# Performance work log

Measured on AMD Instinct MI355X. Metric: run time of the kernel, lower is better.

The kernel has to match this reference:

```python
import jax, jax.numpy as jnp
import numpy as np

D_MODEL = 1024
N_HEADS = 16
MLP_DIM = 4096


def _layernorm(x, g, b, eps=1e-5):
    mu = jnp.mean(x, axis=-1, keepdims=True)
    var = jnp.var(x, axis=-1, keepdims=True)
    return (x - mu) * jax.lax.rsqrt(var + eps) * g + b


def setup_inputs() -> dict:
    key = jax.random.key(0)
    ks = jax.random.split(key, 12)
    B, S, D, F = 2, 2048, D_MODEL, MLP_DIM
    s = 1.0 / np.sqrt(D)
    sf = 1.0 / np.sqrt(F)
    return {
        "x": jax.random.normal(ks[0], (B, S, D), jnp.float32),
        "ln1_g": jnp.ones((D,), jnp.float32),
        "ln1_b": jnp.zeros((D,), jnp.float32),
        "w_q": jax.random.uniform(ks[1], (D, D), jnp.float32, -s, s),
        "w_k": jax.random.uniform(ks[2], (D, D), jnp.float32, -s, s),
        "w_v": jax.random.uniform(ks[3], (D, D), jnp.float32, -s, s),
        "w_o": jax.random.uniform(ks[4], (D, D), jnp.float32, -s, s),
        "b_o": jax.random.uniform(ks[5], (D,), jnp.float32, -s, s),
        "ln2_g": jnp.ones((D,), jnp.float32),
        "ln2_b": jnp.zeros((D,), jnp.float32),
        "w1": jax.random.uniform(ks[6], (D, F), jnp.float32, -s, s),
        "b1": jax.random.uniform(ks[7], (F,), jnp.float32, -s, s),
        "w2": jax.random.uniform(ks[8], (F, D), jnp.float32, -sf, sf),
        "b2": jax.random.uniform(ks[9], (D,), jnp.float32, -sf, sf),
    }


def reference(x, ln1_g, ln1_b, w_q, w_k, w_v, w_o, b_o, ln2_g, ln2_b, w1, b1, w2, b2):
    B, S, D = x.shape
    H = N_HEADS
    hd = D // H
    # --- attention sublayer (pre-LN, residual) ---
    h = _layernorm(x, ln1_g, ln1_b)
    q = (h @ w_q).reshape(B, S, H, hd).transpose(0, 2, 1, 3)  # [B,H,S,hd]
    k = (h @ w_k).reshape(B, S, H, hd).transpose(0, 2, 1, 3)
    v = (h @ w_v).reshape(B, S, H, hd).transpose(0, 2, 1, 3)
    scores = jnp.einsum('bhqd,bhkd->bhqk', q, k) / np.sqrt(hd)  # [B,H,S,S]
    attn = jax.nn.softmax(scores, axis=-1)
    out = jnp.einsum('bhqk,bhkd->bhqd', attn, v)
    out = out.transpose(0, 2, 1, 3).reshape(B, S, D)
    x = out @ w_o + b_o + x
    # --- MLP sublayer (pre-LN, residual) ---
    h = _layernorm(x, ln2_g, ln2_b)
    h = jax.nn.gelu(h @ w1 + b1, approximate=False)
    return h @ w2 + b2 + x
```

## Files before the change

kernel.cpp:

```cpp
#include <hip/hip_runtime.h>
#include <math.h>


typedef __attribute__((ext_vector_type(8))) short s8v;
typedef __attribute__((ext_vector_type(4))) short s4v;
typedef __attribute__((ext_vector_type(4))) float f4v;
typedef __attribute__((ext_vector_type(16))) float f16v;

#define M_ROWS 4096
#define DM 1024
#define FF 4096
#define QKV_LD 3072

__device__ inline short f2bf(float f) {
  unsigned u = __builtin_bit_cast(unsigned, f);
  u += 0x7fff + ((u >> 16) & 1);
  return (short)(u >> 16);
}

__device__ inline void gload_lds16(const void* g, void* lds) {
  __builtin_amdgcn_global_load_lds(
      (const __attribute__((address_space(1))) unsigned*)(uintptr_t)g,
      (__attribute__((address_space(3))) unsigned*)(unsigned)(uintptr_t)lds,
      16, 0, 0);
}

__device__ inline s4v ds_tr16(unsigned off) {
  s4v r;
  asm volatile("ds_read_b64_tr_b16 %0, %1" : "=v"(r) : "v"(off));
  return r;
}

__device__ inline s8v cat8(s4v a, s4v b) {
  return __builtin_shufflevector(a, b, 0, 1, 2, 3, 4, 5, 6, 7);
}

__device__ inline unsigned pkbf(float a, float b) {
  unsigned r;
  asm("v_cvt_pk_bf16_f32 %0, %1, %2" : "=v"(r) : "v"(a), "v"(b));
  return r;
}

__device__ inline float gelu_t(float x) {
  float x3 = x * x * x;
  float z = fmaf(x3, 0.044715f, x) * 1.5957691216f;
  float e = __expf(z);
  float th = fmaf(-2.0f, __frcp_rn(e + 1.0f), 1.0f);
  return 0.5f * x * (1.0f + th);
}

__global__ void wt_kernel(const float* __restrict__ W, short* __restrict__ Wt,
                          int K, int N) {
  __shared__ float tile[32][33];
  int tx = threadIdx.x, ty = threadIdx.y;
  int n0 = blockIdx.x * 32, k0 = blockIdx.y * 32;
#pragma unroll
  for (int i = 0; i < 4; ++i)
    tile[ty + 8 * i][tx] = W[(size_t)(k0 + ty + 8 * i) * N + n0 + tx];
  __syncthreads();
#pragma unroll
  for (int i = 0; i < 4; ++i)
    Wt[(size_t)(n0 + ty + 8 * i) * K + k0 + tx] = f2bf(tile[tx][ty + 8 * i]);
}

__global__ __launch_bounds__(256) void ln_kernel(const float* __restrict__ x,
                                                 const float* __restrict__ g,
                                                 const float* __restrict__ b,
                                                 short* __restrict__ out) {
  int row = blockIdx.x, tid = threadIdx.x;
  const float4* xr = (const float4*)(x + (size_t)row * DM);
  float4 v = xr[tid];
  float s = v.x + v.y + v.z + v.w;
  float q = v.x * v.x + v.y * v.y + v.z * v.z + v.w * v.w;
#pragma unroll
  for (int off = 32; off; off >>= 1) {
    s += __shfl_down(s, off);
    q += __shfl_down(q, off);
  }
  __shared__ float red[8];
  if ((tid & 63) == 0) { red[tid >> 6] = s; red[4 + (tid >> 6)] = q; }
  __syncthreads();
  if (tid == 0) {
    float S = red[0] + red[1] + red[2] + red[3];
    float Q = red[4] + red[5] + red[6] + red[7];
    float mean = S * (1.0f / DM);
    float var = Q * (1.0f / DM) - mean * mean;
    red[0] = mean;
    red[1] = rsqrtf(var + 1e-5f);
  }
  __syncthreads();
  float mean = red[0], rstd = red[1];
  float4 gv = ((const float4*)g)[tid], bv = ((const float4*)b)[tid];
  s4v o;
  o[0] = f2bf((v.x - mean) * rstd * gv.x + bv.x);
  o[1] = f2bf((v.y - mean) * rstd * gv.y + bv.y);
  o[2] = f2bf((v.z - mean) * rstd * gv.z + bv.z);
  o[3] = f2bf((v.w - mean) * rstd * gv.w + bv.w);
  *(s4v*)&out[(size_t)row * DM + tid * 4] = o;
}

template <int EPI>
__global__ __launch_bounds__(256) void gemm_kernel(
    const short* __restrict__ A, const short* __restrict__ Bt,
    const float* __restrict__ bias, const float* __restrict__ res,
    void* __restrict__ Cout, int M, int N, int K) {
  __shared__ short As[2][128 * 64];
  __shared__ short Bs[2][128 * 64];
  int tid = threadIdx.x, lane = tid & 63, wave = tid >> 6;
  int wr = wave >> 1, wc = wave & 1;
  int l16 = lane & 15, lhi = lane >> 4;
  int row0 = blockIdx.y * 128, col0 = blockIdx.x * 128;
  int lrow = lane >> 3, lcol8 = (lane & 7) * 8;

  const f4v fzero = {0.f, 0.f, 0.f, 0.f};
  f4v acc[4][4];
#pragma unroll
  for (int m = 0; m < 4; ++m)
#pragma unroll
    for (int n = 0; n < 4; ++n) acc[m][n] = fzero;

  const int nt = K >> 6;

#pragma unroll
  for (int i = 0; i < 4; ++i) {
    int ch = wave * 4 + i;
    int row = ch * 8 + lrow;
    gload_lds16(&A[(size_t)(row0 + row) * K + lcol8], &As[0][ch * 512]);
    gload_lds16(&Bt[(size_t)(col0 + row) * K + lcol8], &Bs[0][ch * 512]);
  }
  __syncthreads();

  for (int t = 0; t < nt; ++t) {
    int cur = t & 1, nxt = cur ^ 1;
    if (t + 1 < nt) {
      int k1 = (t + 1) << 6;
#pragma unroll
      for (int i = 0; i < 4; ++i) {
        int ch = wave * 4 + i;
        int row = ch * 8 + lrow;
        gload_lds16(&A[(size_t)(row0 + row) * K + k1 + lcol8], &As[nxt][ch * 512]);
        gload_lds16(&Bt[(size_t)(col0 + row) * K + k1 + lcol8], &Bs[nxt][ch * 512]);
      }
    }
#pragma unroll
    for (int kk = 0; kk < 2; ++kk) {
      s8v af[4], bfr[4];
#pragma unroll
      for (int m = 0; m < 4; ++m)
        af[m] = *(const s8v*)&As[cur][(wr * 64 + m * 16 + l16) * 64 + kk * 32 + lhi * 8];
#pragma unroll
      for (int n = 0; n < 4; ++n)
        bfr[n] = *(const s8v*)&Bs[cur][(wc * 64 + n * 16 + l16) * 64 + kk * 32 + lhi * 8];
#pragma unroll
      for (int m = 0; m < 4; ++m)
#pragma unroll
        for (int n = 0; n < 4; ++n)
          acc[m][n] = __builtin_amdgcn_mfma_f32_16x16x32_bf16(af[m], bfr[n],
                                                              acc[m][n], 0, 0, 0);
    }
    __syncthreads();
  }

#pragma unroll
  for (int m = 0; m < 4; ++m)
#pragma unroll
    for (int n = 0; n < 4; ++n)
#pragma unroll
      for (int r = 0; r < 4; ++r) {
        int row = row0 + wr * 64 + m * 16 + lhi * 4 + r;
        int col = col0 + wc * 64 + n * 16 + l16;
        size_t idx = (size_t)row * N + col;
        float v = acc[m][n][r];
        if (EPI == 0) {
          ((short*)Cout)[idx] = f2bf(v);
        } else if (EPI == 1) {
          ((float*)Cout)[idx] = v + bias[col] + res[idx];
        } else {
          ((short*)Cout)[idx] = f2bf(gelu_t(v + bias[col]));
        }
      }
}

__global__ __launch_bounds__(256) void attn_kernel(const short* __restrict__ q,
                                                   const short* __restrict__ k,
                                                   const short* __restrict__ v,
                                                   short* __restrict__ o) {
  __shared__ short Ks[2][64 * 64];
  __shared__ short Vt[2][64 * 64];
  int tid = threadIdx.x, lane = tid & 63, w = tid >> 6;
  int l31 = lane & 31, l15 = lane & 15, h = lane >> 5;
  int qb = blockIdx.x * 128;
  int bh = blockIdx.y;
  int b = bh >> 4, hh = bh & 15;
  const size_t rbase = (size_t)b * 2048 * QKV_LD + (size_t)hh * 64;
  const float S2 = 0.18033688f;

  int ch0 = w * 2, ch1 = w * 2 + 1;
  int krow0 = ch0 * 8 + (lane >> 3), krow1 = ch1 * 8 + (lane >> 3);
  int kcol0 = (((lane & 7) ^ (krow0 & 7)) * 8);
  int kcol1 = (((lane & 7) ^ (krow1 & 7)) * 8);
  int vnb0 = ch0 >> 1, vnb1 = ch1 >> 1;
  int vrem0 = (ch0 & 1) * 64 + lane, vrem1 = (ch1 & 1) * 64 + lane;
  int vkey0 = vrem0 >> 1, vc80 = vrem0 & 1;
  int vkey1 = vrem1 >> 1, vc81 = vrem1 & 1;

#define STAGE_KV(buf, kt)                                                      \
  {                                                                            \
    gload_lds16(&k[rbase + (size_t)((kt) + krow0) * QKV_LD + kcol0],           \
                &Ks[buf][ch0 * 512]);                                          \
    gload_lds16(&k[rbase + (size_t)((kt) + krow1) * QKV_LD + kcol1],           \
                &Ks[buf][ch1 * 512]);                                          \
    gload_lds16(&v[rbase + (size_t)((kt) + vkey0) * QKV_LD + vnb0 * 16 + vc80 * 8], \
                &Vt[buf][ch0 * 512]);                                          \
    gload_lds16(&v[rbase + (size_t)((kt) + vkey1) * QKV_LD + vnb1 * 16 + vc81 * 8], \
                &Vt[buf][ch1 * 512]);                                          \
  }

  int qrow = qb + w * 32 + l31;
  s8v qf[4];
#pragma unroll
  for (int c = 0; c < 4; ++c)
    qf[c] = *(const s8v*)&q[rbase + (size_t)qrow * QKV_LD + c * 16 + h * 8];

  f16v o0, o1;
#pragma unroll
  for (int i = 0; i < 16; ++i) { o0[i] = 0.f; o1[i] = 0.f; }
  float mreg = -3.0e38f, lsum = 0.f;

  STAGE_KV(0, 0);
  __syncthreads();

  for (int t = 0; t < 32; ++t) {
    int cur = t & 1;
    if (t + 1 < 32) STAGE_KV(cur ^ 1, (t + 1) * 64);
    unsigned vtb = (unsigned)(uintptr_t)&Vt[cur][0];

    f16v t0, t1;
#pragma unroll
    for (int i = 0; i < 16; ++i) { t0[i] = 0.f; t1[i] = 0.f; }
    __builtin_amdgcn_s_setprio(1);
#pragma unroll
    for (int c = 0; c < 4; ++c) {
      int slot = ((2 * c + h) ^ (l31 & 7)) * 8;
      s8v k0f = *(const s8v*)&Ks[cur][l31 * 64 + slot];
      s8v k1f = *(const s8v*)&Ks[cur][(32 + l31) * 64 + slot];
      t0 = __builtin_amdgcn_mfma_f32_32x32x16_bf16(k0f, qf[c], t0, 0, 0, 0);
      t1 = __builtin_amdgcn_mfma_f32_32x32x16_bf16(k1f, qf[c], t1, 0, 0, 0);
    }
    __builtin_amdgcn_s_setprio(0);

    float mx[8];
#pragma unroll
    for (int i = 0; i < 8; ++i)
      mx[i] = fmaxf(fmaxf(t0[i], t0[i + 8]), fmaxf(t1[i], t1[i + 8]));
    float rm = fmaxf(fmaxf(fmaxf(mx[0], mx[1]), fmaxf(mx[2], mx[3])),
                     fmaxf(fmaxf(mx[4], mx[5]), fmaxf(mx[6], mx[7])));
    rm = fmaxf(rm, __shfl_xor(rm, 32));
    if (!__all(rm <= mreg + 64.0f)) {
      float newm = fmaxf(mreg, rm);
      float sc = exp2f((mreg - newm) * S2);
      mreg = newm;
#pragma unroll
      for (int i = 0; i < 16; ++i) { o0[i] *= sc; o1[i] *= sc; }
      lsum *= sc;
    }
    float ms2 = mreg * S2;
#pragma unroll
    for (int i = 0; i < 16; ++i) {
      t0[i] = exp2f(fmaf(t0[i], S2, -ms2));
      t1[i] = exp2f(fmaf(t1[i], S2, -ms2));
    }
    float sm[8];
#pragma unroll
    for (int i = 0; i < 8; ++i)
      sm[i] = (t0[i] + t0[i + 8]) + (t1[i] + t1[i + 8]);
    float rs = ((sm[0] + sm[1]) + (sm[2] + sm[3])) +
               ((sm[4] + sm[5]) + (sm[6] + sm[7]));
    rs += __shfl_xor(rs, 32);
    lsum += rs;

    s8v pB[4];
#pragma unroll
    for (int c = 0; c < 4; ++c) {
      int rb = (c & 1) * 8;
      float e0, e1, e2, e3, e4, e5, e6, e7;
      if (c < 2) {
        e0 = t0[rb]; e1 = t0[rb + 1]; e2 = t0[rb + 2]; e3 = t0[rb + 3];
        e4 = t0[rb + 4]; e5 = t0[rb + 5]; e6 = t0[rb + 6]; e7 = t0[rb + 7];
      } else {
        e0 = t1[rb]; e1 = t1[rb + 1]; e2 = t1[rb + 2]; e3 = t1[rb + 3];
        e4 = t1[rb + 4]; e5 = t1[rb + 5]; e6 = t1[rb + 6]; e7 = t1[rb + 7];
      }
      unsigned wA0 = pkbf(e0, e1), wA1 = pkbf(e2, e3);
      unsigned wB0 = pkbf(e4, e5), wB1 = pkbf(e6, e7);
      unsigned s0 = h ? wA0 : wB0, s1 = h ? wA1 : wB1;
      unsigned r0 = __shfl_xor(s0, 32), r1 = __shfl_xor(s1, 32);
      uint4 ww;
      ww.x = h ? r0 : wA0;
      ww.y = h ? r1 : wA1;
      ww.z = h ? wB0 : r0;
      ww.w = h ? wB1 : r1;
      pB[c] = __builtin_bit_cast(s8v, ww);
    }

    s4v va[2][4][2];
#pragma unroll
    for (int db = 0; db < 2; ++db) {
      unsigned base = vtb + (unsigned)(db * 2 + (l31 >> 4)) * 2048 + 2u * l15;
#pragma unroll
      for (int c = 0; c < 4; ++c) {
        unsigned a = base + (unsigned)(c * 512 + h * 256);
        va[db][c][0] = ds_tr16(a);
        va[db][c][1] = ds_tr16(a + 128);
      }
    }
    asm volatile("s_waitcnt lgkmcnt(0)");
    __builtin_amdgcn_sched_barrier(0);
    __builtin_amdgcn_s_setprio(1);
#pragma unroll
    for (int c = 0; c < 4; ++c) {
      o0 = __builtin_amdgcn_mfma_f32_32x32x16_bf16(cat8(va[0][c][0], va[0][c][1]),
                                                   pB[c], o0, 0, 0, 0);
      o1 = __builtin_amdgcn_mfma_f32_32x32x16_bf16(cat8(va[1][c][0], va[1][c][1]),
                                                   pB[c], o1, 0, 0, 0);
    }
    __builtin_amdgcn_s_setprio(0);
    __syncthreads();
  }

  float inv = 1.0f / lsum;
  size_t obase = ((size_t)b * 2048 + qrow) * 1024 + hh * 64;
#pragma unroll
  for (int db = 0; db < 2; ++db)
#pragma unroll
    for (int qq = 0; qq < 4; ++qq) {
      s4v pv;
#pragma unroll
      for (int i = 0; i < 4; ++i) {
        float val = (db == 0 ? o0[qq * 4 + i] : o1[qq * 4 + i]) * inv;
        pv[i] = f2bf(val);
      }
      *(s4v*)&o[obase + db * 32 + qq * 8 + h * 4] = pv;
    }
#undef STAGE_KV
}

extern "C" void kernel_launch(void* const* d_in, const int* in_sizes, int n_in,
                              void* d_out, int out_size, void* d_ws, size_t ws_size,
                              hipStream_t stream) {
  (void)in_sizes; (void)n_in; (void)out_size; (void)ws_size;
  const float* x    = (const float*)d_in[0];
  const float* ln1g = (const float*)d_in[1];
  const float* ln1b = (const float*)d_in[2];
  const float* wq   = (const float*)d_in[3];
  const float* wk   = (const float*)d_in[4];
  const float* wv   = (const float*)d_in[5];
  const float* wo   = (const float*)d_in[6];
  const float* bo   = (const float*)d_in[7];
  const float* ln2g = (const float*)d_in[8];
  const float* ln2b = (const float*)d_in[9];
  const float* w1   = (const float*)d_in[10];
  const float* b1   = (const float*)d_in[11];
  const float* w2   = (const float*)d_in[12];
  const float* b2   = (const float*)d_in[13];
  float* out = (float*)d_out;

  char* ws = (char*)d_ws;
  const size_t MB = 1024 * 1024;
  short* h1   = (short*)(ws);
  short* qkv  = (short*)(ws + 8 * MB);
  short* mid  = (short*)(ws);
  short* at   = (short*)(ws + 32 * MB);
  short* h2   = (short*)(ws + 32 * MB);
  float* x2   = (float*)(ws + 40 * MB);
  short* wqkvT = (short*)(ws + 56 * MB);
  short* wqT  = wqkvT;
  short* wkT  = wqkvT + 1024 * 1024;
  short* wvT  = wqkvT + 2 * 1024 * 1024;
  short* woT  = (short*)(ws + 62 * MB);
  short* w1T  = (short*)(ws + 64 * MB);
  short* w2T  = (short*)(ws + 72 * MB);

  dim3 tb(32, 8);
  wt_kernel<<<dim3(32, 32), tb, 0, stream>>>(wq, wqT, 1024, 1024);
  wt_kernel<<<dim3(32, 32), tb, 0, stream>>>(wk, wkT, 1024, 1024);
  wt_kernel<<<dim3(32, 32), tb, 0, stream>>>(wv, wvT, 1024, 1024);
  wt_kernel<<<dim3(32, 32), tb, 0, stream>>>(wo, woT, 1024, 1024);
  wt_kernel<<<dim3(128, 32), tb, 0, stream>>>(w1, w1T, 1024, 4096);
  wt_kernel<<<dim3(32, 128), tb, 0, stream>>>(w2, w2T, 4096, 1024);

  ln_kernel<<<M_ROWS, 256, 0, stream>>>(x, ln1g, ln1b, h1);

  gemm_kernel<0><<<dim3(24, 32), 256, 0, stream>>>(h1, wqkvT, nullptr, nullptr,
                                                   qkv, M_ROWS, QKV_LD, DM);

  attn_kernel<<<dim3(16, 32), 256, 0, stream>>>(qkv, qkv + 1024, qkv + 2048, at);

  gemm_kernel<1><<<dim3(8, 32), 256, 0, stream>>>(at, woT, bo, x, x2, M_ROWS, DM, DM);

  ln_kernel<<<M_ROWS, 256, 0, stream>>>(x2, ln2g, ln2b, h2);

  gemm_kernel<2><<<dim3(32, 32), 256, 0, stream>>>(h2, w1T, b1, nullptr, mid,
                                                   M_ROWS, FF, DM);

  gemm_kernel<1><<<dim3(8, 32), 256, 0, stream>>>(mid, w2T, b2, x2, out,
                                                  M_ROWS, DM, FF);
}
```

Before: 279.4 us.

## Split attention over key range into two partials with a combine kernel

The attention kernel now splits the 2048-key range into two halves along a new grid z dimension. Each half writes an unnormalized bf16 partial output plus its running max and sum. A new combine kernel merges the two halves with log-sum-exp rescaling. This doubles the attention grid from 512 to 1024 blocks to fill the GPU's compute units better. The cost is an extra launch, extra partial-output traffic, and an extra bf16 rounding of the unnormalized partials.

```diff
diff --git a/kernel.cpp b/kernel.cpp
--- a/kernel.cpp
+++ b/kernel.cpp
@@ -16,6 +16,10 @@
   unsigned u = __builtin_bit_cast(unsigned, f);
   u += 0x7fff + ((u >> 16) & 1);
   return (short)(u >> 16);
+}
+__device__ inline float bf2f(short s) {
+  unsigned u = ((unsigned)(unsigned short)s) << 16;
+  return __builtin_bit_cast(float, u);
 }
 
 __device__ inline void gload_lds16(const void* g, void* lds) {
@@ -184,16 +188,19 @@
 __global__ __launch_bounds__(256) void attn_kernel(const short* __restrict__ q,
                                                    const short* __restrict__ k,
                                                    const short* __restrict__ v,
-                                                   short* __restrict__ o) {
+                                                   short* __restrict__ opart,
+                                                   float2* __restrict__ ml) {
   __shared__ short Ks[2][64 * 64];
   __shared__ short Vt[2][64 * 64];
   int tid = threadIdx.x, lane = tid & 63, w = tid >> 6;
   int l31 = lane & 31, l15 = lane & 15, h = lane >> 5;
   int qb = blockIdx.x * 128;
   int bh = blockIdx.y;
+  int sp = blockIdx.z;
   int b = bh >> 4, hh = bh & 15;
   const size_t rbase = (size_t)b * 2048 * QKV_LD + (size_t)hh * 64;
   const float S2 = 0.18033688f;
+  const int kbase = sp * 1024;
 
   int ch0 = w * 2, ch1 = w * 2 + 1;
   int krow0 = ch0 * 8 + (lane >> 3), krow1 = ch1 * 8 + (lane >> 3);
@@ -227,12 +234,12 @@
   for (int i = 0; i < 16; ++i) { o0[i] = 0.f; o1[i] = 0.f; }
   float mreg = -3.0e38f, lsum = 0.f;
 
-  STAGE_KV(0, 0);
+  STAGE_KV(0, kbase);
   __syncthreads();
 
-  for (int t = 0; t < 32; ++t) {
+  for (int t = 0; t < 16; ++t) {
     int cur = t & 1;
-    if (t + 1 < 32) STAGE_KV(cur ^ 1, (t + 1) * 64);
+    if (t + 1 < 16) STAGE_KV(cur ^ 1, kbase + (t + 1) * 64);
     unsigned vtb = (unsigned)(uintptr_t)&Vt[cur][0];
 
     f16v t0, t1;
@@ -328,21 +335,42 @@
     __syncthreads();
   }
 
-  float inv = 1.0f / lsum;
-  size_t obase = ((size_t)b * 2048 + qrow) * 1024 + hh * 64;
+  size_t rowg = (size_t)b * 2048 + qrow;
+  size_t obase = (size_t)sp * 4096 * 1024 + rowg * 1024 + hh * 64;
 #pragma unroll
   for (int db = 0; db < 2; ++db)
 #pragma unroll
     for (int qq = 0; qq < 4; ++qq) {
       s4v pv;
 #pragma unroll
-      for (int i = 0; i < 4; ++i) {
-        float val = (db == 0 ? o0[qq * 4 + i] : o1[qq * 4 + i]) * inv;
-        pv[i] = f2bf(val);
-      }
-      *(s4v*)&o[obase + db * 32 + qq * 8 + h * 4] = pv;
-    }
+      for (int i = 0; i < 4; ++i)
+        pv[i] = f2bf(db == 0 ? o0[qq * 4 + i] : o1[qq * 4 + i]);
+      *(s4v*)&opart[obase + db * 32 + qq * 8 + h * 4] = pv;
+    }
+  if (h == 0) ml[(size_t)sp * 65536 + rowg * 16 + hh] = make_float2(mreg, lsum);
 #undef STAGE_KV
+}
+
+__global__ __launch_bounds__(256) void attn_combine(const short* __restrict__ op,
+                                                    const float2* __restrict__ ml,
+                                                    short* __restrict__ o) {
+  int row = blockIdx.x, t = threadIdx.x;
+  int head = t >> 4;
+  const float S2 = 0.18033688f;
+  float2 ml0 = ml[(size_t)row * 16 + head];
+  float2 ml1 = ml[65536 + (size_t)row * 16 + head];
+  float M = fmaxf(ml0.x, ml1.x);
+  float a0 = exp2f((ml0.x - M) * S2);
+  float a1 = exp2f((ml1.x - M) * S2);
+  float inv = 1.0f / fmaf(ml0.y, a0, ml1.y * a1);
+  a0 *= inv; a1 *= inv;
+  s4v v0 = *(const s4v*)&op[(size_t)row * 1024 + t * 4];
+  s4v v1 = *(const s4v*)&op[(size_t)4096 * 1024 + row * 1024 + t * 4];
+  s4v pv;
+#pragma unroll
+  for (int i = 0; i < 4; ++i)
+    pv[i] = f2bf(bf2f(v0[i]) * a0 + bf2f(v1[i]) * a1);
+  *(s4v*)&o[(size_t)row * 1024 + t * 4] = pv;
 }
 
 extern "C" void kernel_launch(void* const* d_in, const int* in_sizes, int n_in,
@@ -373,6 +401,8 @@
   short* at   = (short*)(ws + 32 * MB);
   short* h2   = (short*)(ws + 32 * MB);
   float* x2   = (float*)(ws + 40 * MB);
+  short* opart = (short*)(ws + 40 * MB);
+  float2* mlb  = (float2*)(ws);
   short* wqkvT = (short*)(ws + 56 * MB);
   short* wqT  = wqkvT;
   short* wkT  = wqkvT + 1024 * 1024;
@@ -394,7 +424,9 @@
   gemm_kernel<0><<<dim3(24, 32), 256, 0, stream>>>(h1, wqkvT, nullptr, nullptr,
                                                    qkv, M_ROWS, QKV_LD, DM);
 
-  attn_kernel<<<dim3(16, 32), 256, 0, stream>>>(qkv, qkv + 1024, qkv + 2048, at);
+  attn_kernel<<<dim3(16, 32, 2), 256, 0, stream>>>(qkv, qkv + 1024, qkv + 2048,
+                                                   opart, mlb);
+  attn_combine<<<4096, 256, 0, stream>>>(opart, mlb, at);
 
   gemm_kernel<1><<<dim3(8, 32), 256, 0, stream>>>(at, woT, bo, x, x2, M_ROWS, DM, DM);
 
```

After: 287.0 us. 1.03x slower.
